# Performance work log

Hardware: AMD Instinct MI355X
Metric: run time of the kernel (lower is better)

## Reference

```python
import jax, jax.numpy as jnp
import numpy as np

B, N, D_IN = 8, 2048, 1024
H, DH = 4, 256  # num_heads, per-head dim (hidden_dim)
D_OUT = 256


def setup_inputs() -> dict:
    key = jax.random.key(0)
    ks = jax.random.split(key, 5)
    s = 0.02
    return {
        "x": jax.random.normal(ks[0], (B, N, D_IN), dtype=jnp.float32),
        "Wq": jax.random.normal(ks[1], (D_IN, H * DH), dtype=jnp.float32) * s,
        "bq": jnp.zeros((H * DH,), dtype=jnp.float32),
        "Wk": jax.random.normal(ks[2], (D_IN, H * DH), dtype=jnp.float32) * s,
        "bk": jnp.zeros((H * DH,), dtype=jnp.float32),
        "Wv": jax.random.normal(ks[3], (D_IN, H * DH), dtype=jnp.float32) * s,
        "bv": jnp.zeros((H * DH,), dtype=jnp.float32),
        "Wo": jax.random.normal(ks[4], (H * DH, D_OUT), dtype=jnp.float32) * s,
        "bo": jnp.zeros((D_OUT,), dtype=jnp.float32),
    }


def reference(x, Wq, bq, Wk, bk, Wv, bv, Wo, bo):
    b, n, _ = x.shape
    # projections -> [B, N, H, DH]
    q = (x @ Wq + bq).reshape(b, n, H, DH)
    k = (x @ Wk + bk).reshape(b, n, H, DH)
    v = (x @ Wv + bv).reshape(b, n, H, DH)
    scale = 1.0 / jnp.sqrt(jnp.asarray(DH, dtype=x.dtype))
    scores = jnp.einsum("bnhd,bmhd->bhnm", q, k) * scale  # [B,H,N,N]
    weights = jax.nn.softmax(scores, axis=-1)
    attn = jnp.einsum("bhnm,bmhd->bnhd", weights, v)  # [B,N,H,DH]
    attn = attn.reshape(b, n, H * DH)
    return attn @ Wo + bo  # [B, N, D_OUT]
```

## Files before the change

kernel.cpp:

```cpp
#include <hip/hip_runtime.h>
#include <hip/hip_bf16.h>
#include <stdint.h>

typedef __attribute__((ext_vector_type(4))) float  f32x4;
typedef __attribute__((ext_vector_type(4))) float  float4v;
typedef __attribute__((ext_vector_type(8))) short  short8v;
typedef __attribute__((ext_vector_type(4))) short  short4v;
typedef __attribute__((ext_vector_type(8))) unsigned short ushort8v;
typedef __attribute__((ext_vector_type(4))) unsigned short ushort4v;

#define B_   8
#define N_   2048
#define DIN  1024
#define H_   4
#define DH   256
#define QSZ  (B_ * N_ * H_ * DH)

__device__ __forceinline__ unsigned short f2bf(float x) {
  union { float f; unsigned u; } v; v.f = x;
  unsigned r = v.u + 0x7fffu + ((v.u >> 16) & 1u);
  return (unsigned short)(r >> 16);
}

__device__ __forceinline__ short8v pack8(short4v lo, short4v hi) {
  short8v r;
  r[0] = lo[0]; r[1] = lo[1]; r[2] = lo[2]; r[3] = lo[3];
  r[4] = hi[0]; r[5] = hi[1]; r[6] = hi[2]; r[7] = hi[3];
  return r;
}

__device__ __forceinline__ ushort4v ulo4(ushort8v v) {
  ushort4v r; r[0] = v[0]; r[1] = v[1]; r[2] = v[2]; r[3] = v[3]; return r;
}
__device__ __forceinline__ ushort4v uhi4(ushort8v v) {
  ushort4v r; r[0] = v[4]; r[1] = v[5]; r[2] = v[6]; r[3] = v[7]; return r;
}
__device__ __forceinline__ ushort8v umk8(ushort4v a, ushort4v b) {
  ushort8v r;
  r[0] = a[0]; r[1] = a[1]; r[2] = a[2]; r[3] = a[3];
  r[4] = b[0]; r[5] = b[1]; r[6] = b[2]; r[7] = b[3];
  return r;
}

__device__ __forceinline__ unsigned cvtpk(float lo, float hi) {
  unsigned r;
  asm("v_cvt_pk_bf16_f32 %0, %1, %2" : "=v"(r) : "v"(lo), "v"(hi));
  return r;
}

__device__ __forceinline__ void gload_lds16(const void* g, void* l) {
  __builtin_amdgcn_global_load_lds(
      (const __attribute__((address_space(1))) unsigned int*)g,
      (__attribute__((address_space(3))) unsigned int*)l, 16, 0, 0);
}

__global__ __launch_bounds__(256) void prep_wt(
    const float* __restrict__ Wq, const float* __restrict__ Wk,
    const float* __restrict__ Wv, const float* __restrict__ Wo,
    unsigned short* __restrict__ Wt)
{
  __shared__ float Lt[64][68];
  const int tid = threadIdx.x;
  const int c0 = blockIdx.x * 64;
  const int k0 = blockIdx.y * 64;
  const int msel = c0 >> 10;
  const float* src = (msel == 0) ? Wq : (msel == 1) ? Wk : (msel == 2) ? Wv : Wo;
  const int stride = (msel == 3) ? 256 : 1024;
  const int cloc = c0 - msel * 1024;
  #pragma unroll
  for (int p = 0; p < 4; ++p) {
    int kr = p * 16 + (tid >> 4), c4 = (tid & 15) * 4;
    float4v v = *(const float4v*)(src + (size_t)(k0 + kr) * stride + cloc + c4);
    Lt[kr][c4 + 0] = v[0]; Lt[kr][c4 + 1] = v[1];
    Lt[kr][c4 + 2] = v[2]; Lt[kr][c4 + 3] = v[3];
  }
  __syncthreads();
  int n = tid >> 2, kc = (tid & 3) * 16;
  ushort8v h0, h1;
  #pragma unroll
  for (int j = 0; j < 8; ++j) h0[j] = f2bf(Lt[kc + j][n]);
  #pragma unroll
  for (int j = 0; j < 8; ++j) h1[j] = f2bf(Lt[kc + 8 + j][n]);
  unsigned short* dst = Wt + (size_t)(c0 + n) * 1024 + k0 + kc;
  *(ushort8v*)dst = h0;
  *(ushort8v*)(dst + 8) = h1;
}

__global__ __launch_bounds__(512) void qkv_gemm2(
    const float* __restrict__ x, const unsigned short* __restrict__ Wt,
    const float* __restrict__ bq, const float* __restrict__ bk,
    const float* __restrict__ bv, unsigned short* __restrict__ qkv)
{
  __shared__ __align__(16) unsigned short Ab[2][4096];
  __shared__ __align__(16) unsigned short Bb[2][8192];
  const int tid = threadIdx.x;
  const int lane = tid & 63, wid = tid >> 6;
  const int l15 = lane & 15, l4 = lane >> 4;

  const int id = blockIdx.x;
  const int swz = (id & 7) * 192 + (id >> 3);
  const int m0 = (swz / 12) * 128, n0 = (swz % 12) * 256;
  const int wm = (wid >> 2) * 64, wn = (wid & 3) * 64;

  const int arow = tid >> 2, akb = (tid & 3) * 16;
  const int brow1 = wid * 16 + (lane >> 2), bkb = (lane & 3) * 16;
  const float* Abase = x + (size_t)(m0 + arow) * 1024 + (akb >> 1);
  const char* Bg1 = (const char*)Wt + (size_t)(n0 + brow1) * 2048 + bkb;
  const char* Bg2 = Bg1 + 128 * 2048;

  f32x4 acc[4][4] = {};

#define QSTAGE(t, b) do {                                                    \
    float4v f0 = *(const float4v*)(Abase + (t) * 32);                        \
    float4v f1 = *(const float4v*)(Abase + (t) * 32 + 4);                    \
    gload_lds16(Bg1 + (t) * 64, (char*)&Bb[b][0] + wid * 1024);              \
    gload_lds16(Bg2 + (t) * 64, (char*)&Bb[b][0] + 8192 + wid * 1024);       \
    ushort8v hv;                                                             \
    hv[0] = f2bf(f0[0]); hv[1] = f2bf(f0[1]);                                \
    hv[2] = f2bf(f0[2]); hv[3] = f2bf(f0[3]);                                \
    hv[4] = f2bf(f1[0]); hv[5] = f2bf(f1[1]);                                \
    hv[6] = f2bf(f1[2]); hv[7] = f2bf(f1[3]);                                \
    *(ushort8v*)((char*)&Ab[b][0] + tid * 16) = hv;                          \
  } while (0)

  QSTAGE(0, 0);
  __syncthreads();

  for (int t = 0; t < 32; ++t) {
    const int cur = t & 1;
    if (t < 31) QSTAGE(t + 1, cur ^ 1);
    short8v a[4], b[4];
    #pragma unroll
    for (int mf = 0; mf < 4; ++mf)
      a[mf] = *(const short8v*)((const char*)&Ab[cur][0] +
                                (wm + mf * 16 + l15) * 64 + l4 * 16);
    #pragma unroll
    for (int nf = 0; nf < 4; ++nf)
      b[nf] = *(const short8v*)((const char*)&Bb[cur][0] +
                                (wn + nf * 16 + l15) * 64 + l4 * 16);
    #pragma unroll
    for (int mf = 0; mf < 4; ++mf)
      #pragma unroll
      for (int nf = 0; nf < 4; ++nf)
        acc[mf][nf] = __builtin_amdgcn_mfma_f32_16x16x32_bf16(a[mf], b[nf], acc[mf][nf], 0, 0, 0);
    __syncthreads();
  }
#undef QSTAGE

  const int wsel = n0 >> 10;
  const float* bias = (wsel == 0) ? bq : (wsel == 1) ? bk : bv;
  const float scale = (wsel == 0) ? 0.0625f * 1.44269504f : 1.0f;
  unsigned short* dst = qkv + (size_t)wsel * QSZ;
  #pragma unroll
  for (int nf = 0; nf < 4; ++nf) {
    int ncol = n0 + wn + nf * 16 + l15;
    int ncl = ncol & 1023;
    float bv_ = bias[ncl];
    int h = ncl >> 8, d = ncl & 255;
    #pragma unroll
    for (int mf = 0; mf < 4; ++mf)
      #pragma unroll
      for (int e = 0; e < 4; ++e) {
        int mrow = m0 + wm + mf * 16 + l4 * 4 + e;
        int bb = mrow >> 11, nn = mrow & 2047;
        dst[((size_t)(bb * 4 + h) * 2048 + nn) * 256 + d] =
            f2bf((acc[mf][nf][e] + bv_) * scale);
      }
  }
}

__global__ __launch_bounds__(512, 2) void attn_fused(
    unsigned short* __restrict__ qkv)
{
  extern __shared__ __align__(16) char smem[];
  const int tid = threadIdx.x;
  const int lane = tid & 63, wid = tid >> 6;
  const int l15 = lane & 15, l4 = lane >> 4;

  const int id0 = blockIdx.x;
  const int swzb = (id0 & 7) * 32 + (id0 >> 3);
  const int qt = swzb & 7, bh = swzb >> 3;

  const unsigned short* Qh = qkv + (size_t)bh * (N_ * DH);
  const unsigned short* Kh = qkv + (size_t)QSZ + (size_t)bh * (N_ * DH);
  const unsigned short* Vh = qkv + (size_t)2 * QSZ + (size_t)bh * (N_ * DH);

  const int q0 = qt * 256 + wid * 32;
  short8v qf0[8], qf1[8];
  #pragma unroll
  for (int ks = 0; ks < 8; ++ks) {
    const unsigned short* p0 = Qh + (size_t)(q0 + l15) * DH + ks * 32 + l4 * 4;
    const unsigned short* p1 = p0 + 16 * DH;
    qf0[ks] = pack8(*(const short4v*)p0, *(const short4v*)(p0 + 16));
    qf1[ks] = pack8(*(const short4v*)p1, *(const short4v*)(p1 + 16));
  }

  const int skv = tid >> 3, sks = tid & 7;
  const unsigned short* Kg = Kh + (size_t)skv * DH + sks * 32;
  int kdst[4];
  #pragma unroll
  for (int g = 0; g < 4; ++g)
    kdst[g] = (skv * 512 + sks * 64 + g * 16) ^ ((skv & 7) << 4);

  int vgoff[4];
  #pragma unroll
  for (int j = 0; j < 4; ++j) {
    int u = j * 512 + wid * 64 + lane;
    vgoff[j] = ((u >> 1) & 63) * 512 + (u >> 7) * 32 + (u & 1) * 16;
  }

  f32x4 ot0[16] = {}, ot1[16] = {};
  float m0r = -1.0e30f, m1r = -1.0e30f, l0p = 0.0f, l1p = 0.0f;

  ushort8v kin0, kin1, kin2, kin3;

#define KBUF(b) (smem + (b) * 32768)
#define VBUF(b) (smem + 65536 + (b) * 32768)

#define KISSUE(t) do {                                                       \
    const unsigned short* kp = Kg + (size_t)(t) * (64 * DH);                 \
    kin0 = *(const ushort8v*)(kp);                                           \
    kin1 = *(const ushort8v*)(kp + 8);                                       \
    kin2 = *(const ushort8v*)(kp + 16);                                      \
    kin3 = *(const ushort8v*)(kp + 24);                                      \
  } while (0)

#define KWRITE(b) do {                                                       \
    char* kb = KBUF(b);                                                      \
    *(ushort8v*)(kb + kdst[0]) = umk8(ulo4(kin0), ulo4(kin2));               \
    *(ushort8v*)(kb + kdst[1]) = umk8(uhi4(kin0), uhi4(kin2));               \
    *(ushort8v*)(kb + kdst[2]) = umk8(ulo4(kin1), ulo4(kin3));               \
    *(ushort8v*)(kb + kdst[3]) = umk8(uhi4(kin1), uhi4(kin3));               \
  } while (0)

#define VISSUE(t, b) do {                                                    \
    const char* vg = (const char*)Vh + (size_t)(t) * 32768;                  \
    _Pragma("unroll")                                                        \
    for (int j = 0; j < 4; ++j)                                              \
      gload_lds16(vg + vgoff[j], VBUF(b) + j * 8192 + wid * 1024);           \
  } while (0)

#define TRD(dst, off)                                                        \
    asm volatile("ds_read_b64_tr_b16 %0, %1" : "=v"(dst)                     \
                 : "v"(vb + (unsigned)(off)))

#define ISSUE8(R, g) do {                                                    \
    TRD(R##0, (2*(g)) * 2048 + 0);    TRD(R##1, (2*(g)) * 2048 + 512);       \
    TRD(R##2, (2*(g)) * 2048 + 1024); TRD(R##3, (2*(g)) * 2048 + 1536);      \
    TRD(R##4, (2*(g)+1) * 2048 + 0);    TRD(R##5, (2*(g)+1) * 2048 + 512);   \
    TRD(R##6, (2*(g)+1) * 2048 + 1024); TRD(R##7, (2*(g)+1) * 2048 + 1536);  \
  } while (0)

#define BMF __builtin_amdgcn_mfma_f32_16x16x32_bf16
#define MFMA8(R, g) do {                                                     \
    __builtin_amdgcn_s_setprio(1);                                           \
    ot0[2*(g)]   = BMF(pack8(R##0, R##1), pbA0, ot0[2*(g)],   0, 0, 0);      \
    ot1[2*(g)]   = BMF(pack8(R##0, R##1), pbA1, ot1[2*(g)],   0, 0, 0);      \
    ot0[2*(g)]   = BMF(pack8(R##2, R##3), pbB0, ot0[2*(g)],   0, 0, 0);      \
    ot1[2*(g)]   = BMF(pack8(R##2, R##3), pbB1, ot1[2*(g)],   0, 0, 0);      \
    ot0[2*(g)+1] = BMF(pack8(R##4, R##5), pbA0, ot0[2*(g)+1], 0, 0, 0);      \
    ot1[2*(g)+1] = BMF(pack8(R##4, R##5), pbA1, ot1[2*(g)+1], 0, 0, 0);      \
    ot0[2*(g)+1] = BMF(pack8(R##6, R##7), pbB0, ot0[2*(g)+1], 0, 0, 0);      \
    ot1[2*(g)+1] = BMF(pack8(R##6, R##7), pbB1, ot1[2*(g)+1], 0, 0, 0);      \
    __builtin_amdgcn_s_setprio(0);                                           \
  } while (0)

#define PVSTEP(C, Nx, g, last) do {                                          \
    if (!(last)) {                                                           \
      ISSUE8(Nx, (g) + 1);                                                   \
      asm volatile("s_waitcnt lgkmcnt(8)" ::: "memory");                     \
    } else {                                                                 \
      asm volatile("s_waitcnt lgkmcnt(0)" ::: "memory");                     \
    }                                                                        \
    __builtin_amdgcn_sched_barrier(0);                                       \
    MFMA8(C, g);                                                             \
  } while (0)

#define MX4(v) fmaxf(fmaxf(v[0], v[1]), fmaxf(v[2], v[3]))

  union UPK { unsigned u[4]; short8v v; };

#define EXPPACK(sA, sB, m, lacc, pdst) do {                                  \
    float e0 = exp2f(sA[0] - m), e1 = exp2f(sA[1] - m);                      \
    float e2 = exp2f(sA[2] - m), e3 = exp2f(sA[3] - m);                      \
    float e4 = exp2f(sB[0] - m), e5 = exp2f(sB[1] - m);                      \
    float e6 = exp2f(sB[2] - m), e7 = exp2f(sB[3] - m);                      \
    lacc += ((e0 + e1) + (e2 + e3)) + ((e4 + e5) + (e6 + e7));               \
    UPK up;                                                                  \
    up.u[0] = cvtpk(e0, e1); up.u[1] = cvtpk(e2, e3);                        \
    up.u[2] = cvtpk(e4, e5); up.u[3] = cvtpk(e6, e7);                        \
    pdst = up.v;                                                             \
  } while (0)

  KISSUE(0);
  VISSUE(0, 0);
  KWRITE(0);
  __syncthreads();

  for (int t = 0; t < 32; ++t) {
    const int cur = t & 1;
    if (t < 31) { KISSUE(t + 1); VISSUE(t + 1, cur ^ 1); }

    const char* Kc = KBUF(cur);
    const int swzk = (l15 & 7) << 4;
    f32x4 st00 = {0,0,0,0}, st01 = {0,0,0,0}, st10 = {0,0,0,0}, st11 = {0,0,0,0};
    f32x4 st20 = {0,0,0,0}, st21 = {0,0,0,0}, st30 = {0,0,0,0}, st31 = {0,0,0,0};
    __builtin_amdgcn_s_setprio(1);
    #pragma unroll
    for (int ks = 0; ks < 8; ++ks) {
      const char* pr = Kc + l15 * 512 + ((ks * 64 + l4 * 16) ^ swzk);
      short8v af0 = *(const short8v*)(pr);
      short8v af1 = *(const short8v*)(pr + 8192);
      short8v af2 = *(const short8v*)(pr + 16384);
      short8v af3 = *(const short8v*)(pr + 24576);
      st00 = BMF(af0, qf0[ks], st00, 0, 0, 0);
      st01 = BMF(af0, qf1[ks], st01, 0, 0, 0);
      st10 = BMF(af1, qf0[ks], st10, 0, 0, 0);
      st11 = BMF(af1, qf1[ks], st11, 0, 0, 0);
      st20 = BMF(af2, qf0[ks], st20, 0, 0, 0);
      st21 = BMF(af2, qf1[ks], st21, 0, 0, 0);
      st30 = BMF(af3, qf0[ks], st30, 0, 0, 0);
      st31 = BMF(af3, qf1[ks], st31, 0, 0, 0);
    }
    __builtin_amdgcn_s_setprio(0);

    if (t < 31) KWRITE(cur ^ 1);

    float tmax0 = fmaxf(fmaxf(MX4(st00), MX4(st10)), fmaxf(MX4(st20), MX4(st30)));
    float tmax1 = fmaxf(fmaxf(MX4(st01), MX4(st11)), fmaxf(MX4(st21), MX4(st31)));
    tmax0 = fmaxf(tmax0, __shfl_xor(tmax0, 16));
    tmax1 = fmaxf(tmax1, __shfl_xor(tmax1, 16));
    tmax0 = fmaxf(tmax0, __shfl_xor(tmax0, 32));
    tmax1 = fmaxf(tmax1, __shfl_xor(tmax1, 32));
    if (__any(tmax0 > m0r + 11.54f)) {
      float mn = fmaxf(m0r, tmax0), al = exp2f(m0r - mn);
      l0p *= al;
      #pragma unroll
      for (int df = 0; df < 16; ++df) ot0[df] *= al;
      m0r = mn;
    }
    if (__any(tmax1 > m1r + 11.54f)) {
      float mn = fmaxf(m1r, tmax1), al = exp2f(m1r - mn);
      l1p *= al;
      #pragma unroll
      for (int df = 0; df < 16; ++df) ot1[df] *= al;
      m1r = mn;
    }

    const unsigned vb = (unsigned)(uintptr_t)(VBUF(cur)) + lane * 8;
    short4v A0, A1, A2, A3, A4, A5, A6, A7, B0, B1, B2, B3, B4, B5, B6, B7;
    ISSUE8(A, 0);

    short8v pbA0, pbB0, pbA1, pbB1;
    EXPPACK(st00, st10, m0r, l0p, pbA0);
    EXPPACK(st20, st30, m0r, l0p, pbB0);
    EXPPACK(st01, st11, m1r, l1p, pbA1);
    EXPPACK(st21, st31, m1r, l1p, pbB1);

    PVSTEP(A, B, 0, 0); PVSTEP(B, A, 1, 0);
    PVSTEP(A, B, 2, 0); PVSTEP(B, A, 3, 0);
    PVSTEP(A, B, 4, 0); PVSTEP(B, A, 5, 0);
    PVSTEP(A, B, 6, 0); PVSTEP(B, A, 7, 1);

    __syncthreads();
  }

  unsigned short* Oq = (unsigned short*)Qh;
  {
    float ps = l0p;
    ps += __shfl_xor(ps, 16);
    ps += __shfl_xor(ps, 32);
    float inv = 1.0f / ps;
    size_t base = (size_t)(q0 + l15) * DH;
    #pragma unroll
    for (int df = 0; df < 16; ++df) {
      ushort4v o;
      #pragma unroll
      for (int e = 0; e < 4; ++e) o[e] = f2bf(ot0[df][e] * inv);
      *(ushort4v*)&Oq[base + df * 16 + l4 * 4] = o;
    }
  }
  {
    float ps = l1p;
    ps += __shfl_xor(ps, 16);
    ps += __shfl_xor(ps, 32);
    float inv = 1.0f / ps;
    size_t base = (size_t)(q0 + 16 + l15) * DH;
    #pragma unroll
    for (int df = 0; df < 16; ++df) {
      ushort4v o;
      #pragma unroll
      for (int e = 0; e < 4; ++e) o[e] = f2bf(ot1[df][e] * inv);
      *(ushort4v*)&Oq[base + df * 16 + l4 * 4] = o;
    }
  }
#undef KISSUE
#undef KWRITE
#undef VISSUE
#undef TRD
#undef ISSUE8
#undef MFMA8
#undef PVSTEP
#undef MX4
#undef EXPPACK
#undef KBUF
#undef VBUF
#undef BMF
}

__global__ __launch_bounds__(512) void out_gemm2(
    const unsigned short* __restrict__ Aq, const unsigned short* __restrict__ WoT,
    const float* __restrict__ bo, float* __restrict__ out)
{
  __shared__ __align__(16) unsigned short Ab[2][4096];
  __shared__ __align__(16) unsigned short Bb[2][8192];
  const int tid = threadIdx.x;
  const int lane = tid & 63, wid = tid >> 6;
  const int l15 = lane & 15, l4 = lane >> 4;
  const int m0 = blockIdx.x * 128;
  const int wm = (wid >> 2) * 64, wn = (wid & 3) * 64;

  const int arow = wid * 16 + (lane >> 2), akb = (lane & 3) * 16;
  const int bb = m0 >> 11;
  const int qrow = (m0 & 2047) + arow;
  const char* Bg1 = (const char*)WoT + (size_t)arow * 2048 + akb;
  const char* Bg2 = Bg1 + 128 * 2048;

  f32x4 acc[4][4] = {};

#define OSTAGE(t, b) do {                                                    \
    int h = (t) >> 3, d0 = (((t) & 7) * 32) + (akb >> 1);                    \
    gload_lds16(Aq + ((size_t)(bb * 4 + h) * 2048 + qrow) * 256 + d0,        \
                (char*)&Ab[b][0] + wid * 1024);                              \
    gload_lds16(Bg1 + (t) * 64, (char*)&Bb[b][0] + wid * 1024);              \
    gload_lds16(Bg2 + (t) * 64, (char*)&Bb[b][0] + 8192 + wid * 1024);       \
  } while (0)

  OSTAGE(0, 0);
  __syncthreads();

  for (int t = 0; t < 32; ++t) {
    const int cur = t & 1;
    if (t < 31) OSTAGE(t + 1, cur ^ 1);
    short8v a[4], b[4];
    #pragma unroll
    for (int mf = 0; mf < 4; ++mf)
      a[mf] = *(const short8v*)((const char*)&Ab[cur][0] +
                                (wm + mf * 16 + l15) * 64 + l4 * 16);
    #pragma unroll
    for (int nf = 0; nf < 4; ++nf)
      b[nf] = *(const short8v*)((const char*)&Bb[cur][0] +
                                (wn + nf * 16 + l15) * 64 + l4 * 16);
    #pragma unroll
    for (int mf = 0; mf < 4; ++mf)
      #pragma unroll
      for (int nf = 0; nf < 4; ++nf)
        acc[mf][nf] = __builtin_amdgcn_mfma_f32_16x16x32_bf16(a[mf], b[nf], acc[mf][nf], 0, 0, 0);
    __syncthreads();
  }
#undef OSTAGE

  #pragma unroll
  for (int nf = 0; nf < 4; ++nf) {
    int ncol = wn + nf * 16 + l15;
    float bv_ = bo[ncol];
    #pragma unroll
    for (int mf = 0; mf < 4; ++mf)
      #pragma unroll
      for (int e = 0; e < 4; ++e) {
        int mrow = m0 + wm + mf * 16 + l4 * 4 + e;
        out[(size_t)mrow * 256 + ncol] = acc[mf][nf][e] + bv_;
      }
  }
}

extern "C" void kernel_launch(void* const* d_in, const int* in_sizes, int n_in,
                              void* d_out, int out_size, void* d_ws, size_t ws_size,
                              hipStream_t stream) {
  const float* x  = (const float*)d_in[0];
  const float* Wq = (const float*)d_in[1];
  const float* bq = (const float*)d_in[2];
  const float* Wk = (const float*)d_in[3];
  const float* bk = (const float*)d_in[4];
  const float* Wv = (const float*)d_in[5];
  const float* bv = (const float*)d_in[6];
  const float* Wo = (const float*)d_in[7];
  const float* bo = (const float*)d_in[8];

  unsigned short* qkvbuf = (unsigned short*)d_ws;
  unsigned short* Wt     = qkvbuf + (size_t)3 * QSZ;
  float* out = (float*)d_out;

  prep_wt  <<<dim3(52, 16), 256, 0, stream>>>(Wq, Wk, Wv, Wo, Wt);
  qkv_gemm2<<<dim3(1536),   512, 0, stream>>>(x, Wt, bq, bk, bv, qkvbuf);
  attn_fused<<<dim3(256),   512, 131072, stream>>>(qkvbuf);
  out_gemm2<<<dim3(128),    512, 0, stream>>>(qkvbuf, Wt + (size_t)3072 * 1024, bo, out);
}
```

Measured before the change: 398.9 us.

## Store V transposed from QKV GEMM and drop LDS transpose reads in PV

```diff
diff --git a/kernel.cpp b/kernel.cpp
--- a/kernel.cpp
+++ b/kernel.cpp
@@ -149,23 +149,41 @@
 
   const int wsel = n0 >> 10;
   const float* bias = (wsel == 0) ? bq : (wsel == 1) ? bk : bv;
-  const float scale = (wsel == 0) ? 0.0625f * 1.44269504f : 1.0f;
-  unsigned short* dst = qkv + (size_t)wsel * QSZ;
-  #pragma unroll
-  for (int nf = 0; nf < 4; ++nf) {
-    int ncol = n0 + wn + nf * 16 + l15;
-    int ncl = ncol & 1023;
-    float bv_ = bias[ncl];
-    int h = ncl >> 8, d = ncl & 255;
-    #pragma unroll
-    for (int mf = 0; mf < 4; ++mf)
-      #pragma unroll
-      for (int e = 0; e < 4; ++e) {
-        int mrow = m0 + wm + mf * 16 + l4 * 4 + e;
-        int bb = mrow >> 11, nn = mrow & 2047;
-        dst[((size_t)(bb * 4 + h) * 2048 + nn) * 256 + d] =
-            f2bf((acc[mf][nf][e] + bv_) * scale);
+  if (wsel == 2) {
+    unsigned short* vt = qkv + (size_t)2 * QSZ;
+    #pragma unroll
+    for (int nf = 0; nf < 4; ++nf) {
+      int ncl = (n0 + wn + nf * 16 + l15) & 1023;
+      float bv_ = bias[ncl];
+      int h = ncl >> 8, d = ncl & 255;
+      #pragma unroll
+      for (int mf = 0; mf < 4; ++mf) {
+        int mrow0 = m0 + wm + mf * 16 + l4 * 4;
+        int bb = mrow0 >> 11, nn0 = mrow0 & 2047;
+        ushort4v o;
+        #pragma unroll
+        for (int e = 0; e < 4; ++e) o[e] = f2bf(acc[mf][nf][e] + bv_);
+        *(ushort4v*)&vt[((size_t)((bb * 4 + h) * 256 + d)) * 2048 + nn0] = o;
       }
+    }
+  } else {
+    const float scale = (wsel == 0) ? 0.0625f * 1.44269504f : 1.0f;
+    unsigned short* dst = qkv + (size_t)wsel * QSZ;
+    #pragma unroll
+    for (int nf = 0; nf < 4; ++nf) {
+      int ncl = (n0 + wn + nf * 16 + l15) & 1023;
+      float bv_ = bias[ncl];
+      int h = ncl >> 8, d = ncl & 255;
+      #pragma unroll
+      for (int mf = 0; mf < 4; ++mf)
+        #pragma unroll
+        for (int e = 0; e < 4; ++e) {
+          int mrow = m0 + wm + mf * 16 + l4 * 4 + e;
+          int bb = mrow >> 11, nn = mrow & 2047;
+          dst[((size_t)(bb * 4 + h) * 2048 + nn) * 256 + d] =
+              f2bf((acc[mf][nf][e] + bv_) * scale);
+        }
+    }
   }
 }
 
@@ -183,7 +201,7 @@
 
   const unsigned short* Qh = qkv + (size_t)bh * (N_ * DH);
   const unsigned short* Kh = qkv + (size_t)QSZ + (size_t)bh * (N_ * DH);
-  const unsigned short* Vh = qkv + (size_t)2 * QSZ + (size_t)bh * (N_ * DH);
+  const unsigned short* Vt = qkv + (size_t)2 * QSZ + (size_t)bh * (N_ * DH);
 
   const int q0 = qt * 256 + wid * 32;
   short8v qf0[8], qf1[8];
@@ -205,9 +223,16 @@
   int vgoff[4];
   #pragma unroll
   for (int j = 0; j < 4; ++j) {
-    int u = j * 512 + wid * 64 + lane;
-    vgoff[j] = ((u >> 1) & 63) * 512 + (u >> 7) * 32 + (u & 1) * 16;
-  }
+    int r = j * 64 + wid * 8 + (lane >> 3);
+    int u = lane & 7;
+    vgoff[j] = r * 4096 + ((u ^ (r & 7)) << 4);
+  }
+
+  const int rsw = (l15 & 7);
+  const int vb00 = l15 * 128 + (((0 + 0 + (l4 >> 1)) ^ rsw) << 4) + (l4 & 1) * 8;
+  const int vb01 = l15 * 128 + (((0 + 2 + (l4 >> 1)) ^ rsw) << 4) + (l4 & 1) * 8;
+  const int vb10 = l15 * 128 + (((4 + 0 + (l4 >> 1)) ^ rsw) << 4) + (l4 & 1) * 8;
+  const int vb11 = l15 * 128 + (((4 + 2 + (l4 >> 1)) ^ rsw) << 4) + (l4 & 1) * 8;
 
   f32x4 ot0[16] = {}, ot1[16] = {};
   float m0r = -1.0e30f, m1r = -1.0e30f, l0p = 0.0f, l1p = 0.0f;
@@ -234,48 +259,13 @@
   } while (0)
 
 #define VISSUE(t, b) do {                                                    \
-    const char* vg = (const char*)Vh + (size_t)(t) * 32768;                  \
+    const char* vg = (const char*)Vt + (size_t)(t) * 128;                    \
     _Pragma("unroll")                                                        \
     for (int j = 0; j < 4; ++j)                                              \
       gload_lds16(vg + vgoff[j], VBUF(b) + j * 8192 + wid * 1024);           \
   } while (0)
 
-#define TRD(dst, off)                                                        \
-    asm volatile("ds_read_b64_tr_b16 %0, %1" : "=v"(dst)                     \
-                 : "v"(vb + (unsigned)(off)))
-
-#define ISSUE8(R, g) do {                                                    \
-    TRD(R##0, (2*(g)) * 2048 + 0);    TRD(R##1, (2*(g)) * 2048 + 512);       \
-    TRD(R##2, (2*(g)) * 2048 + 1024); TRD(R##3, (2*(g)) * 2048 + 1536);      \
-    TRD(R##4, (2*(g)+1) * 2048 + 0);    TRD(R##5, (2*(g)+1) * 2048 + 512);   \
-    TRD(R##6, (2*(g)+1) * 2048 + 1024); TRD(R##7, (2*(g)+1) * 2048 + 1536);  \
-  } while (0)
-
 #define BMF __builtin_amdgcn_mfma_f32_16x16x32_bf16
-#define MFMA8(R, g) do {                                                     \
-    __builtin_amdgcn_s_setprio(1);                                           \
-    ot0[2*(g)]   = BMF(pack8(R##0, R##1), pbA0, ot0[2*(g)],   0, 0, 0);      \
-    ot1[2*(g)]   = BMF(pack8(R##0, R##1), pbA1, ot1[2*(g)],   0, 0, 0);      \
-    ot0[2*(g)]   = BMF(pack8(R##2, R##3), pbB0, ot0[2*(g)],   0, 0, 0);      \
-    ot1[2*(g)]   = BMF(pack8(R##2, R##3), pbB1, ot1[2*(g)],   0, 0, 0);      \
-    ot0[2*(g)+1] = BMF(pack8(R##4, R##5), pbA0, ot0[2*(g)+1], 0, 0, 0);      \
-    ot1[2*(g)+1] = BMF(pack8(R##4, R##5), pbA1, ot1[2*(g)+1], 0, 0, 0);      \
-    ot0[2*(g)+1] = BMF(pack8(R##6, R##7), pbB0, ot0[2*(g)+1], 0, 0, 0);      \
-    ot1[2*(g)+1] = BMF(pack8(R##6, R##7), pbB1, ot1[2*(g)+1], 0, 0, 0);      \
-    __builtin_amdgcn_s_setprio(0);                                           \
-  } while (0)
-
-#define PVSTEP(C, Nx, g, last) do {                                          \
-    if (!(last)) {                                                           \
-      ISSUE8(Nx, (g) + 1);                                                   \
-      asm volatile("s_waitcnt lgkmcnt(8)" ::: "memory");                     \
-    } else {                                                                 \
-      asm volatile("s_waitcnt lgkmcnt(0)" ::: "memory");                     \
-    }                                                                        \
-    __builtin_amdgcn_sched_barrier(0);                                       \
-    MFMA8(C, g);                                                             \
-  } while (0)
-
 #define MX4(v) fmaxf(fmaxf(v[0], v[1]), fmaxf(v[2], v[3]))
 
   union UPK { unsigned u[4]; short8v v; };
@@ -347,20 +337,26 @@
       m1r = mn;
     }
 
-    const unsigned vb = (unsigned)(uintptr_t)(VBUF(cur)) + lane * 8;
-    short4v A0, A1, A2, A3, A4, A5, A6, A7, B0, B1, B2, B3, B4, B5, B6, B7;
-    ISSUE8(A, 0);
-
     short8v pbA0, pbB0, pbA1, pbB1;
     EXPPACK(st00, st10, m0r, l0p, pbA0);
     EXPPACK(st20, st30, m0r, l0p, pbB0);
     EXPPACK(st01, st11, m1r, l1p, pbA1);
     EXPPACK(st21, st31, m1r, l1p, pbB1);
 
-    PVSTEP(A, B, 0, 0); PVSTEP(B, A, 1, 0);
-    PVSTEP(A, B, 2, 0); PVSTEP(B, A, 3, 0);
-    PVSTEP(A, B, 4, 0); PVSTEP(B, A, 5, 0);
-    PVSTEP(A, B, 6, 0); PVSTEP(B, A, 7, 1);
+    const char* Vc = VBUF(cur);
+    __builtin_amdgcn_s_setprio(1);
+    #pragma unroll
+    for (int df = 0; df < 16; ++df) {
+      short4v r0 = *(const short4v*)(Vc + vb00 + df * 2048);
+      short4v r1 = *(const short4v*)(Vc + vb01 + df * 2048);
+      short4v r2 = *(const short4v*)(Vc + vb10 + df * 2048);
+      short4v r3 = *(const short4v*)(Vc + vb11 + df * 2048);
+      ot0[df] = BMF(pack8(r0, r1), pbA0, ot0[df], 0, 0, 0);
+      ot1[df] = BMF(pack8(r0, r1), pbA1, ot1[df], 0, 0, 0);
+      ot0[df] = BMF(pack8(r2, r3), pbB0, ot0[df], 0, 0, 0);
+      ot1[df] = BMF(pack8(r2, r3), pbB1, ot1[df], 0, 0, 0);
+    }
+    __builtin_amdgcn_s_setprio(0);
 
     __syncthreads();
   }
@@ -397,10 +393,6 @@
 #undef KISSUE
 #undef KWRITE
 #undef VISSUE
-#undef TRD
-#undef ISSUE8
-#undef MFMA8
-#undef PVSTEP
 #undef MX4
 #undef EXPPACK
 #undef KBUF
```

New measurement: 413.0 us. 1.04x slower.
